# Performance work log

Hardware: AMD Instinct MI355X
Metric: run time of the kernel (lower is better)

Reference implementation:

```python
import jax, jax.numpy as jnp
import numpy as np

B, N, DIM = 4, 2048, 768
HEADS, DH, DEPTH = 12, 64, 4
W = 35                     # hard-coded window size
P = DIM // 2               # window-embedding proj dim
V4 = DIM // 4              # window-embedding value dim
PB = DIM // 4              # dynamic pos-bias MLP width
FF = DIM * 4
NEG = float(np.finfo(np.float32).max)


def setup_inputs() -> dict:
    key = jax.random.key(0)
    ks = iter(jax.random.split(key, 32))
    r = lambda shape: jax.random.normal(next(ks), shape, jnp.float32) * 0.02
    return dict(
        x=jax.random.normal(next(ks), (B, N, DIM), jnp.float32),
        mask=jnp.zeros((B, N), bool),
        ln1_g=jnp.ones((DEPTH, DIM)), ln1_b=jnp.zeros((DEPTH, DIM)),
        qkv_W=r((DEPTH, DIM, 3 * HEADS * DH)),
        temp=jnp.full((DEPTH,), 15.5, jnp.float32),
        we_lin_W=r((DEPTH, DIM, P)), we_q_W=r((DEPTH, P, P)),
        we_k_W=r((DEPTH, DIM, P)), we_v_W=r((DEPTH, DIM, V4)),
        we_bos=jnp.zeros((DEPTH, V4)), we_scale=jnp.ones((DEPTH,)),
        out_W=r((DEPTH, DIM + V4, DIM)),
        ln2_g=jnp.ones((DEPTH, DIM)), ln2_b=jnp.zeros((DEPTH, DIM)),
        glu_W=r((DEPTH, DIM, 2 * FF)), glu_b=jnp.zeros((DEPTH, 2 * FF)),
        ffo_W=r((DEPTH, FF, DIM)), ffo_b=jnp.zeros((DEPTH, DIM)),
        pb_W1=r((1, PB)), pb_b1=jnp.zeros((PB,)),
        pb_W2=r((PB, PB)), pb_b2=jnp.zeros((PB,)),
        pb_W3=r((PB, HEADS)), pb_b3=jnp.zeros((HEADS,)),
    )


def _ln(x, g, b):
    m = x.mean(-1, keepdims=True)
    v = ((x - m) ** 2).mean(-1, keepdims=True)
    return (x - m) * jax.lax.rsqrt(v + 1e-5) * g + b


def _l2norm(t):
    # matches F.normalize(p=2, dim=-1): x / max(||x||, 1e-12)
    return t / jnp.maximum(jnp.linalg.norm(t, axis=-1, keepdims=True), 1e-12)


def _pos_bias(n, W1, b1, W2, b2, W3, b3):
    # DynamicPositionBias(dim=PB, depth=2): Linear->ReLU, Linear->ReLU, Linear
    pos = jnp.arange(-n + 1, n, dtype=jnp.float32)[:, None]          # (2n-1, 1)
    h = jax.nn.relu(pos @ W1 + b1)
    h = jax.nn.relu(h @ W2 + b2)
    out = h @ W3 + b3                                                # (2n-1, H)
    idx = jnp.arange(n)[:, None] - jnp.arange(n)[None, :] + n - 1    # (n, n)
    return jnp.transpose(out[idx], (2, 0, 1))                        # (H, n, n)


def _sinu(n, scale):
    # ScaledSinuEmbedding over proj dim P
    inv = 1.0 / (10000.0 ** (jnp.arange(0, P, 2, dtype=jnp.float32) / P))
    s = jnp.arange(n, dtype=jnp.float32)[:, None] * inv[None, :]
    return jnp.concatenate([jnp.sin(s), jnp.cos(s)], -1) * scale     # (n, P)


def _forward(x, mask, ln1_g, ln1_b, qkv_W, temp, we_lin_W, we_q_W, we_k_W,
             we_v_W, we_bos, we_scale, out_W, ln2_g, ln2_b, glu_W, glu_b,
             ffo_W, ffo_b, pb_W1, pb_b1, pb_W2, pb_b2, pb_W3, pb_b3):
    Bz, Nn, _ = x.shape
    pad = (-Nn) % W
    nw = (Nn + pad) // W
    bias = _pos_bias(W, pb_W1, pb_b1, pb_W2, pb_b2, pb_W3, pb_b3)    # (H, W, W)
    causal = jnp.triu(jnp.ones((W, W), bool), 1)
    mpad = jnp.concatenate([mask, jnp.ones((Bz, pad), bool)], 1).reshape(Bz, nw, W)
    valid = ~mpad                                                    # (B, w, n)
    amask = ~(valid[:, None, :, :, None] & valid[:, None, :, None, :]) | causal
    we_mask = mpad[:, :, None, :]                                    # (B, w, 1, n)
    lengths = jnp.maximum(valid.sum(-1), 1).astype(jnp.float32)[..., None, None]
    sinu35 = _sinu(W, 1.0)                                           # (W, P)

    for l in range(DEPTH):
        # ---- PreNorm + windowed cosine attention ----
        h = _ln(x, ln1_g[l], ln1_b[l])
        hp = jnp.concatenate([h, jnp.zeros((Bz, pad, DIM), h.dtype)], 1)
        hp = hp.reshape(Bz, nw, W, DIM)
        qkv = (hp @ qkv_W[l]).reshape(Bz, nw, W, HEADS, DH, 3)
        q, k, v = (jnp.transpose(qkv[..., i], (0, 3, 1, 2, 4)) for i in range(3))
        q, k = _l2norm(q), _l2norm(k)
        dots = jnp.einsum('bhwid,bhwjd->bhwij', q, k) * temp[l] + bias[None, :, None]
        dots = jnp.where(amask, -NEG, dots)
        attn = jax.nn.softmax(dots, axis=-1)
        o = jnp.einsum('bhwij,bhwjd->bhwid', attn, v)
        o = jnp.transpose(o, (0, 2, 3, 1, 4)).reshape(Bz, nw, W, HEADS * DH)
        # ---- window_embeddings: pooled prev-window embedding attention ----
        we = jnp.where(mpad[..., None], 0.0, o) @ we_lin_W[l]         # (B,w,n,P)
        we = jax.nn.relu(we.sum(-2, keepdims=True) / lengths)        # (B,w,1,P)
        wq = we @ we_q_W[l]
        k2 = o @ we_k_W[l] + sinu35 * we_scale[l]
        v2 = o @ we_v_W[l]
        d2 = jnp.einsum('bwid,bwjd->bwij', wq, k2) * (P ** -0.5)
        d2 = jnp.where(we_mask, -NEG, d2)
        o2 = jnp.einsum('bwij,bwjd->bwid', jax.nn.softmax(d2, -1), v2)  # (B,w,1,V4)
        bos = jnp.broadcast_to(we_bos[l], (Bz, 1, 1, V4))
        o2 = jnp.concatenate([bos, o2], 1)[:, :-1]                   # shift by one window
        o = jnp.concatenate([o, jnp.broadcast_to(o2, (Bz, nw, W, V4))], -1)
        o = (o @ out_W[l]).reshape(Bz, nw * W, DIM)[:, :Nn]
        x = x + o
        # ---- PreNorm + GLU feed-forward ----
        h2 = _ln(x, ln2_g[l], ln2_b[l])
        a, g = jnp.split(h2 @ glu_W[l] + glu_b[l], 2, axis=-1)
        x = x + ((a * jax.nn.silu(g)) @ ffo_W[l] + ffo_b[l])
    return x


def reference(x, mask, ln1_g, ln1_b, qkv_W, temp, we_lin_W, we_q_W, we_k_W,
              we_v_W, we_bos, we_scale, out_W, ln2_g, ln2_b, glu_W, glu_b,
              ffo_W, ffo_b, pb_W1, pb_b1, pb_W2, pb_b2, pb_W3, pb_b3):
    return _forward(x, mask, ln1_g, ln1_b, qkv_W, temp, we_lin_W, we_q_W,
                    we_k_W, we_v_W, we_bos, we_scale, out_W, ln2_g, ln2_b,
                    glu_W, glu_b, ffo_W, ffo_b, pb_W1, pb_b1, pb_W2, pb_b2,
                    pb_W3, pb_b3)
```

## Files before the change

### kernel.cpp

```cpp
#include <hip/hip_runtime.h>
#include <hip/hip_bf16.h>
#include <cstddef>
#include <cstdint>

#define B_ 4
#define N_ 2048
#define DIM_ 768
#define HEADS_ 12
#define DH_ 64
#define DEPTH_ 4
#define W_ 35
#define P_ 384
#define V4_ 192
#define FF_ 3072
#define NW_ 59
#define NPB_ (NW_*W_)
#define NTOK_ (B_*N_)
#define NWB_ (B_*NW_)
#define NTP_ (NWB_*W_)
#define NTPA_ 8448
#define NEG_ 3.402823466e+38f

typedef __bf16 bf16x8 __attribute__((ext_vector_type(8)));
typedef float  f32x4  __attribute__((ext_vector_type(4)));

#define GLOAD16(g, l) __builtin_amdgcn_global_load_lds( \
    (const __attribute__((address_space(1))) uint32_t*)(g), \
    (__attribute__((address_space(3))) uint32_t*)(l), 16, 0, 0)


__global__ __launch_bounds__(192) void posbias1_k(
    const float* __restrict__ W1, const float* __restrict__ b1,
    const float* __restrict__ W2, const float* __restrict__ b2,
    const float* __restrict__ W3, const float* __restrict__ b3,
    float* __restrict__ outk)
{
    __shared__ float h1[192];
    __shared__ float h2[192];
    int i = blockIdx.x;
    int tid = threadIdx.x;
    float pos = (float)(i - 34);
    h1[tid] = fmaxf(pos*W1[tid] + b1[tid], 0.f);
    __syncthreads();
    float s = b2[tid];
    for (int k=0;k<192;k++) s += h1[k]*W2[k*192+tid];
    h2[tid] = fmaxf(s, 0.f);
    __syncthreads();
    if (tid < 12){
        float o = b3[tid];
        for (int k=0;k<192;k++) o += h2[k]*W3[k*12+tid];
        outk[i*12+tid] = o;
    }
}

__global__ void posbias2_k(const float* __restrict__ outk, float* __restrict__ bias)
{
    int e = threadIdx.x + blockIdx.x*blockDim.x;
    if (e >= HEADS_*W_*W_) return;
    int h=e/(W_*W_); int rem=e%(W_*W_); int i=rem/W_; int j=rem%W_;
    bias[e] = outk[(i-j+W_-1)*12 + h];
}

__global__ void sinu_k(float* __restrict__ sinu)
{
    int i = blockIdx.x;
    int k = threadIdx.x;
    float inv = powf(10000.f, -(float)k/192.f);
    float s = (float)i * inv;
    sinu[i*P_ + k]       = sinf(s);
    sinu[i*P_ + 192 + k] = cosf(s);
}

__global__ void len_k(const unsigned char* __restrict__ mask, float* __restrict__ len)
{
    int bw = threadIdx.x + blockIdx.x*blockDim.x;
    if (bw >= NWB_) return;
    int b = bw / NW_, w = bw % NW_;
    int cnt = 0;
    for (int t=0;t<W_;t++){
        int g = w*W_ + t;
        if (g < N_ && mask[b*N_+g]==0) cnt++;
    }
    len[bw] = fmaxf((float)cnt, 1.f);
}

__global__ __launch_bounds__(256) void pack_k(
    const float* __restrict__ W, __bf16* __restrict__ Bp,
    int N, int Ncov, int Nld, size_t lsW, size_t lsB, int qkvperm, int ncol0)
{
    int n = blockIdx.x*256 + threadIdx.x;
    int k8 = blockIdx.y, l = blockIdx.z;
    if (n >= Ncov) return;
    bf16x8 v;
    if (n < N){
        int sn = n;
        if (qkvperm){ int s = n/768, hd = n - s*768; sn = hd*3 + s; }
        const float* w = W + lsW*l + (size_t)k8*8*N + sn;
        #pragma unroll
        for (int e=0;e<8;e++) v[e] = (__bf16)w[(size_t)e*N];
    } else {
        #pragma unroll
        for (int e=0;e<8;e++) v[e] = (__bf16)0.f;
    }
    *(bf16x8*)(Bp + lsB*l + ((size_t)k8*Nld + ncol0 + n)*8) = v;
}

__global__ __launch_bounds__(256) void ln_k(
    const float* __restrict__ x, const float* __restrict__ g,
    const float* __restrict__ b, __bf16* __restrict__ out,
    const float* __restrict__ o2p, int padded)
{
    int r = blockIdx.x;
    int tid = threadIdx.x;
    int lane = tid & 63, wave = tid >> 6;
    int row = r; bool real = true;
    if (padded){
        int bb = r / NPB_, n = r % NPB_;
        if (n >= N_) real = false;
        row = bb*N_ + n;
    }
    float v0=0,v1=0,v2=0;
    if (real){
        const float* xr = x + (size_t)row*DIM_;
        v0 = xr[tid]; v1 = xr[tid+256]; v2 = xr[tid+512];
        if (o2p){
            int bb = row / N_, nn = row % N_;
            const float* op = o2p + (size_t)(bb*NW_ + nn/W_)*DIM_;
            v0 += op[tid]; v1 += op[tid+256]; v2 += op[tid+512];
        }
    }
    float s1 = v0+v1+v2;
    float s2 = v0*v0+v1*v1+v2*v2;
    #pragma unroll
    for (int off=32; off; off>>=1){
        s1 += __shfl_xor(s1, off);
        s2 += __shfl_xor(s2, off);
    }
    __shared__ float a1[4], a2[4];
    if (lane==0){ a1[wave]=s1; a2[wave]=s2; }
    __syncthreads();
    s1 = a1[0]+a1[1]+a1[2]+a1[3];
    s2 = a2[0]+a2[1]+a2[2]+a2[3];
    float m   = s1 * (1.f/768.f);
    float var = s2 * (1.f/768.f) - m*m;
    float inv = rsqrtf(var + 1e-5f);
    __bf16* o = out + (size_t)r*DIM_;
    if (!real){ o[tid]=(__bf16)0.f; o[tid+256]=(__bf16)0.f; o[tid+512]=(__bf16)0.f; return; }
    o[tid]     = (__bf16)((v0-m)*inv*g[tid]     + b[tid]);
    o[tid+256] = (__bf16)((v1-m)*inv*g[tid+256] + b[tid+256]);
    o[tid+512] = (__bf16)((v2-m)*inv*g[tid+512] + b[tid+512]);
}

template<int EPI, bool DUAL, int BM>
__global__ __launch_bounds__(256) void mgemm_k(
    const __bf16* __restrict__ A, const __bf16* __restrict__ Bp,
    float* __restrict__ Cf, __bf16* __restrict__ Cb, float* __restrict__ Cf2,
    float* __restrict__ Cx,
    const float* __restrict__ bias, const float* __restrict__ extra,
    const float* __restrict__ scale_ptr,
    int M, int K, int Nc, int Nld, int Cld)
{
    constexpr int BN = DUAL ? 64 : 128;
    constexpr int RS = BM / 2;
    constexpr int MF = RS / 16;
    constexpr int NF = (BN/2) / 16;
    constexpr int AS = BM * 32;
    constexpr int BS = BN * 32;
    constexpr int ALD = BM / 64;
    constexpr int NL  = ALD + 2;
    __shared__ alignas(16) __bf16 As[3*AS];
    __shared__ alignas(16) __bf16 Bs[3*BS];
    __shared__ alignas(16) __bf16 Gs[DUAL ? 3*BS : 16];
    const int tid = threadIdx.x;
    const int lane = tid & 63, wave = tid >> 6;
    const int wr = wave >> 1, wc = wave & 1;
    const int m0 = blockIdx.y*BM;
    const int n0 = blockIdx.x*BN;
    const int lk = lane >> 4, lr = lane & 15;
    f32x4 acc[MF][NF] = {};
    f32x4 acc2[DUAL?MF:1][NF] = {};

    const __bf16* aP[ALD];
    int aO[ALD];
    #pragma unroll
    for (int q=0;q<ALD;q++){
        int i = tid + q*256;
        int r = i & (BM-1), k8 = i / BM;
        aP[q] = A + (size_t)(m0+r)*K + k8*8;
        aO[q] = i*8;
    }
    const __bf16* bP[2];
    int bO[2];
    if constexpr (!DUAL){
        #pragma unroll
        for (int q=0;q<2;q++){
            int i = tid + q*256;
            int n = i & 127, k8 = i >> 7;
            bP[q] = Bp + ((size_t)k8*Nld + n0 + n)*8;
            bO[q] = i*8;
        }
    } else {
        int n = tid & 63, k8 = tid >> 6;
        bP[0] = Bp + ((size_t)k8*Nld + n0 + n)*8;
        bP[1] = bP[0] + (size_t)FF_*8;
        bO[0] = tid*8;
        bO[1] = tid*8;
    }
    const size_t bStep = (size_t)Nld*32;

    auto stage = [&](int wb){
        #pragma unroll
        for (int q=0;q<ALD;q++)
            GLOAD16(aP[q], As + wb*AS + aO[q]);
        if constexpr (!DUAL){
            GLOAD16(bP[0], Bs + wb*BS + bO[0]);
            GLOAD16(bP[1], Bs + wb*BS + bO[1]);
        } else {
            GLOAD16(bP[0], Bs + wb*BS + bO[0]);
            GLOAD16(bP[1], Gs + wb*BS + bO[1]);
        }
        #pragma unroll
        for (int q=0;q<ALD;q++) aP[q] += 32;
        bP[0] += bStep; bP[1] += bStep;
    };

    const int nk = K >> 5;
    stage(0);
    stage(1);
    int rb = 0;
    for (int t = 0; t < nk; ++t){
        if (t == nk-1)              asm volatile("s_waitcnt vmcnt(0)" ::: "memory");
        else if constexpr (NL == 3) asm volatile("s_waitcnt vmcnt(3)" ::: "memory");
        else                        asm volatile("s_waitcnt vmcnt(4)" ::: "memory");
        __builtin_amdgcn_s_barrier();
        __builtin_amdgcn_sched_barrier(0);
        if (t + 2 < nk){
            int wb = rb + 2; if (wb >= 3) wb -= 3;
            stage(wb);
        }
        const __bf16* as = As + rb*AS + (size_t)(lk*BM + wr*RS + lr)*8;
        const __bf16* bs = Bs + rb*BS + (size_t)(lk*BN + wc*(BN/2) + lr)*8;
        bf16x8 af[MF], bfr[NF];
        #pragma unroll
        for (int m=0;m<MF;m++) af[m] = *(const bf16x8*)(as + m*128);
        #pragma unroll
        for (int n=0;n<NF;n++) bfr[n] = *(const bf16x8*)(bs + n*128);
        __builtin_amdgcn_s_setprio(1);
        #pragma unroll
        for (int m=0;m<MF;m++)
            #pragma unroll
            for (int n=0;n<NF;n++)
                acc[m][n] = __builtin_amdgcn_mfma_f32_16x16x32_bf16(af[m], bfr[n], acc[m][n], 0,0,0);
        if constexpr (DUAL){
            const __bf16* gs = Gs + rb*BS + (size_t)(lk*BN + wc*(BN/2) + lr)*8;
            bf16x8 gfr[NF];
            #pragma unroll
            for (int n=0;n<NF;n++) gfr[n] = *(const bf16x8*)(gs + n*128);
            #pragma unroll
            for (int m=0;m<MF;m++)
                #pragma unroll
                for (int n=0;n<NF;n++)
                    acc2[m][n] = __builtin_amdgcn_mfma_f32_16x16x32_bf16(af[m], gfr[n], acc2[m][n], 0,0,0);
        }
        __builtin_amdgcn_s_setprio(0);
        rb++; if (rb >= 3) rb = 0;
    }

    const int lq = lane >> 4;
    #pragma unroll
    for (int m=0;m<MF;m++){
        #pragma unroll
        for (int r=0;r<4;r++){
            int row = m0 + wr*RS + m*16 + lq*4 + r;
            if (row >= M) continue;
            #pragma unroll
            for (int n=0;n<NF;n++){
                int col = n0 + wc*(BN/2) + n*16 + lr;
                if (col >= Nc) continue;
                float v = acc[m][n][r];
                if (EPI==1){
                    Cb[(size_t)row*Cld + col] = (__bf16)v;
                } else if (EPI==3){
                    int bb = row / N_, nn = row % N_;
                    int bw = bb*NW_ + nn/W_;
                    Cf[(size_t)row*Cld + col] += v + bias[col]
                        + extra[(size_t)bw*DIM_ + col];
                } else if (EPI==4){
                    float a_ = v + bias[col];
                    float g_ = acc2[m][n][r] + bias[col + FF_];
                    Cb[(size_t)row*Cld + col] = (__bf16)(a_ * (g_ / (1.f + expf(-g_))));
                } else if (EPI==8){
                    if (col < P_){
                        int tt = (row % NPB_) % W_;
                        Cf[(size_t)row*P_ + col] = v + extra[tt*P_ + col]*scale_ptr[0];
                    } else if (col < 576){
                        Cf2[(size_t)row*V4_ + (col - P_)] = v;
                    } else {
                        int bb = row / NPB_, nn = row % NPB_;
                        if (nn < N_)
                            Cx[(size_t)(bb*N_ + nn)*DIM_ + (col - 576)] += v;
                    }
                }
            }
        }
    }
}

__global__ __launch_bounds__(256) void gemm0_k(
    const float* __restrict__ A, const float* __restrict__ Bw,
    float* __restrict__ C, int M, int K, int Nc, int ldb)
{
    __shared__ float As[16][65];
    __shared__ float Bs[16][65];
    const int m0 = blockIdx.y*64, n0 = blockIdx.x*64;
    const int tid = threadIdx.x;
    const int ty = tid>>4, tx = tid&15;
    float acc[4][4] = {};
    for (int k0=0; k0<K; k0+=16){
        #pragma unroll
        for (int i=0;i<4;i++){
            int e = tid + i*256;
            int m = e>>4, kk = e&15;
            int mg = m0+m;
            As[kk][m] = (mg < M) ? A[(size_t)mg*K + k0+kk] : 0.f;
        }
        #pragma unroll
        for (int i=0;i<4;i++){
            int e = tid + i*256;
            int kk = e>>6, n = e&63;
            Bs[kk][n] = Bw[(size_t)(k0+kk)*ldb + n0+n];
        }
        __syncthreads();
        #pragma unroll
        for (int kk=0;kk<16;kk++){
            float a[4], bv[4];
            #pragma unroll
            for (int i=0;i<4;i++) a[i] = As[kk][ty*4+i];
            #pragma unroll
            for (int j=0;j<4;j++) bv[j] = Bs[kk][tx*4+j];
            #pragma unroll
            for (int i=0;i<4;i++)
                #pragma unroll
                for (int j=0;j<4;j++) acc[i][j] += a[i]*bv[j];
        }
        __syncthreads();
    }
    #pragma unroll
    for (int i=0;i<4;i++){
        int mg = m0 + ty*4 + i;
        if (mg >= M) continue;
        #pragma unroll
        for (int j=0;j<4;j++){
            int c = n0 + tx*4 + j;
            if (c >= Nc) continue;
            C[(size_t)mg*Nc + c] = acc[i][j];
        }
    }
}

__global__ __launch_bounds__(256) void attn_k(
    const __bf16* __restrict__ qkv, const unsigned char* __restrict__ mask,
    const float* __restrict__ bias, const float* __restrict__ temp_p,
    __bf16* __restrict__ obuf, float* __restrict__ osum)
{
    int bid = blockIdx.x;
    int w = bid % NW_;
    int h = (bid / NW_) % HEADS_;
    int b = bid / (NW_*HEADS_);
    int tid = threadIdx.x;
    __shared__ float qs[W_*DH_], ks[W_*DH_], vs[W_*DH_];
    __shared__ float sc[W_*W_];
    __shared__ float osacc[4][64];
    __shared__ int vf[W_];
    int bw = b*NW_ + w;
    int rbase = bw*W_;
    for (int e=tid; e<W_*DH_; e+=256){
        int t=e>>6, d=e&63;
        size_t idx = (size_t)(rbase+t)*(3*DIM_) + h*DH_ + d;
        qs[e]=(float)qkv[idx];
        ks[e]=(float)qkv[idx+768];
        vs[e]=(float)qkv[idx+1536];
    }
    if (tid < W_){
        int g = w*W_ + tid;
        vf[tid] = (g < N_) && (mask[b*N_+g]==0);
    }
    __syncthreads();
    for (int e=tid; e<2*W_; e+=256){
        float* src = (e<W_)? qs : ks;
        int t = (e<W_)? e : e-W_;
        float s=0;
        for (int d=0;d<DH_;d++){ float v=src[t*DH_+d]; s+=v*v; }
        float inv = 1.f / fmaxf(sqrtf(s), 1e-12f);
        for (int d=0;d<DH_;d++) src[t*DH_+d] *= inv;
    }
    __syncthreads();
    float temp = temp_p[0];
    for (int e=tid; e<W_*W_; e+=256){
        int i=e/W_, j=e%W_;
        float s;
        if (!vf[i] || !vf[j] || j>i) s = -NEG_;
        else {
            float acc=0;
            for (int d=0;d<DH_;d++) acc += qs[i*DH_+d]*ks[j*DH_+d];
            s = acc*temp + bias[(h*W_+i)*W_+j];
        }
        sc[e]=s;
    }
    __syncthreads();
    if (tid < W_){
        int i=tid;
        float mx=-INFINITY;
        for (int j=0;j<W_;j++) mx=fmaxf(mx, sc[i*W_+j]);
        float sum=0;
        for (int j=0;j<W_;j++){ float e_=expf(sc[i*W_+j]-mx); sc[i*W_+j]=e_; sum+=e_; }
        float inv=1.f/sum;
        for (int j=0;j<W_;j++) sc[i*W_+j]*=inv;
    }
    __syncthreads();
    int wavei = tid >> 6, d = tid & 63;
    float psum = 0.f;
    for (int i = wavei; i < W_; i += 4){
        float s=0;
        for (int j=0;j<W_;j++) s += sc[i*W_+j]*vs[j*DH_+d];
        obuf[(size_t)(rbase+i)*DIM_ + h*DH_ + d] = (__bf16)s;
        if (vf[i]) psum += s;
    }
    osacc[wavei][d] = psum;
    __syncthreads();
    if (tid < 64)
        osum[(size_t)bw*DIM_ + h*DH_ + tid] =
            osacc[0][tid]+osacc[1][tid]+osacc[2][tid]+osacc[3][tid];
}

__global__ __launch_bounds__(384) void wefuse_k(
    const float* __restrict__ osum, const float* __restrict__ we_lin,
    const float* __restrict__ we_q, const float* __restrict__ k2,
    const float* __restrict__ v2, const unsigned char* __restrict__ mask,
    const float* __restrict__ len, float* __restrict__ o2)
{
    int bw = blockIdx.x;
    int b = bw / NW_, w = bw % NW_;
    int tid = threadIdx.x;
    __shared__ float osr[768], werr[384], wqr[384], pp[W_];
    osr[tid]     = osum[(size_t)bw*DIM_ + tid];
    osr[tid+384] = osum[(size_t)bw*DIM_ + tid + 384];
    __syncthreads();
    float invlen = 1.f / len[bw];
    float s = 0;
    for (int k=0;k<768;k++) s += osr[k]*we_lin[(size_t)k*P_ + tid];
    werr[tid] = fmaxf(s*invlen, 0.f);
    __syncthreads();
    s = 0;
    for (int k=0;k<384;k++) s += werr[k]*we_q[(size_t)k*P_ + tid];
    wqr[tid] = s;
    __syncthreads();
    if (tid < W_){
        int g = w*W_ + tid;
        bool val = (g < N_) && (mask[b*N_+g]==0);
        float sv = -NEG_;
        if (val){
            float acc=0;
            const float* kr = k2 + (size_t)(bw*W_+tid)*P_;
            for (int c=0;c<P_;c++) acc += wqr[c]*kr[c];
            sv = acc * 0.05103103630798287f;
        }
        pp[tid]=sv;
    }
    __syncthreads();
    if (tid==0){
        float mx=-INFINITY;
        for (int j=0;j<W_;j++) mx=fmaxf(mx,pp[j]);
        float sum=0;
        for (int j=0;j<W_;j++){ float e=expf(pp[j]-mx); pp[j]=e; sum+=e; }
        float inv=1.f/sum;
        for (int j=0;j<W_;j++) pp[j]*=inv;
    }
    __syncthreads();
    if (tid < V4_){
        float sv=0;
        for (int j=0;j<W_;j++) sv += pp[j]*v2[(size_t)(bw*W_+j)*V4_ + tid];
        o2[(size_t)bw*V4_ + tid] = sv;
    }
}

__global__ void o2shift_k(const float* __restrict__ o2, const float* __restrict__ bos,
                          float* __restrict__ o2u)
{
    int e = threadIdx.x + blockIdx.x*blockDim.x;
    if (e >= NWB_*V4_) return;
    int bw = e / V4_, c = e % V4_;
    int w = bw % NW_;
    o2u[e] = (w==0) ? bos[c] : o2[e - V4_];
}


extern "C" void kernel_launch(void* const* d_in, const int* in_sizes, int n_in,
                              void* d_out, int out_size, void* d_ws, size_t ws_size,
                              hipStream_t stream)
{
    const float* x       = (const float*)d_in[0];
    const unsigned char* mask = (const unsigned char*)d_in[1];
    const float* ln1_g   = (const float*)d_in[2];
    const float* ln1_b   = (const float*)d_in[3];
    const float* qkv_W   = (const float*)d_in[4];
    const float* temp    = (const float*)d_in[5];
    const float* we_lin_W= (const float*)d_in[6];
    const float* we_q_W  = (const float*)d_in[7];
    const float* we_k_W  = (const float*)d_in[8];
    const float* we_v_W  = (const float*)d_in[9];
    const float* we_bos  = (const float*)d_in[10];
    const float* we_scale= (const float*)d_in[11];
    const float* out_W   = (const float*)d_in[12];
    const float* ln2_g   = (const float*)d_in[13];
    const float* ln2_b   = (const float*)d_in[14];
    const float* glu_W   = (const float*)d_in[15];
    const float* glu_b   = (const float*)d_in[16];
    const float* ffo_W   = (const float*)d_in[17];
    const float* ffo_b   = (const float*)d_in[18];
    const float* pb_W1   = (const float*)d_in[19];
    const float* pb_b1   = (const float*)d_in[20];
    const float* pb_W2   = (const float*)d_in[21];
    const float* pb_b2   = (const float*)d_in[22];
    const float* pb_W3   = (const float*)d_in[23];
    const float* pb_b3   = (const float*)d_in[24];

    float* xc = (float*)d_out;

    char* p = (char*)d_ws;
    auto alloc = [&](size_t bytes)->char* {
        char* r = p; p += (bytes + 255) & ~(size_t)255; return r;
    };
    float* f_outk = (float*)alloc((size_t)69*12*4);
    float* f_bias = (float*)alloc((size_t)HEADS_*W_*W_*4);
    float* f_sinu = (float*)alloc((size_t)W_*P_*4);
    float* f_len  = (float*)alloc((size_t)NWB_*4);
    float* f_osum = (float*)alloc((size_t)NWB_*DIM_*4);
    float* f_o2   = (float*)alloc((size_t)NWB_*V4_*4);
    float* f_o2u  = (float*)alloc((size_t)NWB_*V4_*4);
    float* f_o2p  = (float*)alloc((size_t)NWB_*DIM_*4);
    __bf16* w_qkv = (__bf16*)alloc((size_t)DEPTH_*96*2304*8*2);
    __bf16* w_kvo = (__bf16*)alloc((size_t)DEPTH_*96*1408*8*2);
    __bf16* w_glu = (__bf16*)alloc((size_t)DEPTH_*96*6144*8*2);
    __bf16* w_ffo = (__bf16*)alloc((size_t)DEPTH_*384*768*8*2);
    char* arena = p;
    __bf16* f_hpad = (__bf16*)alloc((size_t)NTPA_*DIM_*2);
    __bf16* f_qkvb = (__bf16*)alloc((size_t)NTP_*3*DIM_*2);
    __bf16* f_obuf = (__bf16*)alloc((size_t)NTPA_*DIM_*2);
    float*  f_k2   = (float*)alloc((size_t)NTP_*P_*4);
    float*  f_v2   = (float*)alloc((size_t)NTP_*V4_*4);
    __bf16* f_h2 = (__bf16*)arena;
    __bf16* f_ag = (__bf16*)(arena + (((size_t)NTOK_*DIM_*2 + 255) & ~(size_t)255));
    (void)ws_size; (void)in_sizes; (void)n_in; (void)out_size;

    hipMemcpyAsync(xc, x, (size_t)NTOK_*DIM_*sizeof(float),
                   hipMemcpyDeviceToDevice, stream);
    posbias1_k<<<69,192,0,stream>>>(pb_W1,pb_b1,pb_W2,pb_b2,pb_W3,pb_b3,f_outk);
    posbias2_k<<<(HEADS_*W_*W_+255)/256,256,0,stream>>>(f_outk, f_bias);
    sinu_k<<<W_,192,0,stream>>>(f_sinu);
    len_k<<<1,256,0,stream>>>(mask, f_len);
    pack_k<<<dim3(9,96,DEPTH_),256,0,stream>>>(qkv_W, w_qkv, 2304, 2304, 2304,
        (size_t)768*2304, (size_t)96*2304*8, 1, 0);
    pack_k<<<dim3(2,96,DEPTH_),256,0,stream>>>(we_k_W, w_kvo, 384, 384, 1408,
        (size_t)768*384, (size_t)96*1408*8, 0, 0);
    pack_k<<<dim3(1,96,DEPTH_),256,0,stream>>>(we_v_W, w_kvo, 192, 192, 1408,
        (size_t)768*192, (size_t)96*1408*8, 0, 384);
    pack_k<<<dim3(4,96,DEPTH_),256,0,stream>>>(out_W, w_kvo, 768, 832, 1408,
        (size_t)960*768, (size_t)96*1408*8, 0, 576);
    pack_k<<<dim3(24,96,DEPTH_),256,0,stream>>>(glu_W, w_glu, 6144, 6144, 6144,
        (size_t)768*6144, (size_t)96*6144*8, 0, 0);
    pack_k<<<dim3(3,384,DEPTH_),256,0,stream>>>(ffo_W, w_ffo, 768, 768, 768,
        (size_t)3072*768, (size_t)384*768*8, 0, 0);

    for (int l=0;l<DEPTH_;l++){
        ln_k<<<NTP_,256,0,stream>>>(xc, ln1_g+l*DIM_, ln1_b+l*DIM_, f_hpad,
            nullptr, 1);
        mgemm_k<1,false,128><<<dim3(18,65),256,0,stream>>>(f_hpad,
            w_qkv + (size_t)l*96*2304*8, nullptr, f_qkvb, nullptr, nullptr,
            nullptr, nullptr, nullptr, NTP_, DIM_, 3*DIM_, 3*DIM_, 3*DIM_);
        attn_k<<<B_*HEADS_*NW_,256,0,stream>>>(f_qkvb, mask, f_bias, temp+l,
            f_obuf, f_osum);
        mgemm_k<8,false,64><<<dim3(11,130),256,0,stream>>>(f_obuf,
            w_kvo + (size_t)l*96*1408*8, f_k2, nullptr, f_v2, xc,
            nullptr, f_sinu, we_scale+l, NTP_, DIM_, 1344, 1408, 0);
        wefuse_k<<<NWB_,384,0,stream>>>(f_osum, we_lin_W + (size_t)l*DIM_*P_,
            we_q_W + (size_t)l*P_*P_, f_k2, f_v2, mask, f_len, f_o2);
        o2shift_k<<<(NWB_*V4_+255)/256,256,0,stream>>>(f_o2, we_bos+l*V4_, f_o2u);
        gemm0_k<<<dim3(12,4),256,0,stream>>>(f_o2u,
            out_W + (size_t)l*(DIM_+V4_)*DIM_ + (size_t)DIM_*DIM_,
            f_o2p, NWB_, V4_, DIM_, DIM_);

        ln_k<<<NTOK_,256,0,stream>>>(xc, ln2_g+l*DIM_, ln2_b+l*DIM_, f_h2,
            f_o2p, 0);
        mgemm_k<4,true,128><<<dim3(48,64),256,0,stream>>>(f_h2,
            w_glu + (size_t)l*96*6144*8, nullptr, f_ag, nullptr, nullptr,
            glu_b + (size_t)l*2*FF_, nullptr, nullptr,
            NTOK_, DIM_, FF_, 2*FF_, FF_);
        mgemm_k<3,false,64><<<dim3(6,128),256,0,stream>>>(f_ag,
            w_ffo + (size_t)l*384*768*8, xc, nullptr, nullptr, nullptr,
            ffo_b + (size_t)l*DIM_, f_o2p, nullptr,
            NTOK_, FF_, DIM_, DIM_, DIM_);
    }
}
```

Measured before the change: 2.216 ms.

## Enlarge GEMM M-tiles, fold o2 shift into gemm0, pad attention smem

Doubles the BM tile of the KV/out, GLU and FFO GEMMs, halving grid rows so each block reuses its B tile across more rows. A new vmcnt branch handles the extra loads per stage that the larger tile needs. The separate o2shift kernel and its buffer are removed, and gemm0 now reads the shifted o2/bos rows directly. Attention q/k shared arrays get a row stride of 65 to avoid LDS bank conflicts. The larger tiles lower the block count and may hurt occupancy or wave balance on the GPU.

```diff
diff --git a/kernel.cpp b/kernel.cpp
--- a/kernel.cpp
+++ b/kernel.cpp
@@ -20,6 +20,7 @@
 #define NTP_ (NWB_*W_)
 #define NTPA_ 8448
 #define NEG_ 3.402823466e+38f
+#define QLD_ 65
 
 typedef __bf16 bf16x8 __attribute__((ext_vector_type(8)));
 typedef float  f32x4  __attribute__((ext_vector_type(4)));
@@ -231,7 +232,8 @@
     for (int t = 0; t < nk; ++t){
         if (t == nk-1)              asm volatile("s_waitcnt vmcnt(0)" ::: "memory");
         else if constexpr (NL == 3) asm volatile("s_waitcnt vmcnt(3)" ::: "memory");
-        else                        asm volatile("s_waitcnt vmcnt(4)" ::: "memory");
+        else if constexpr (NL == 4) asm volatile("s_waitcnt vmcnt(4)" ::: "memory");
+        else                        asm volatile("s_waitcnt vmcnt(6)" ::: "memory");
         __builtin_amdgcn_s_barrier();
         __builtin_amdgcn_sched_barrier(0);
         if (t + 2 < nk){
@@ -307,8 +309,9 @@
 }
 
 __global__ __launch_bounds__(256) void gemm0_k(
-    const float* __restrict__ A, const float* __restrict__ Bw,
-    float* __restrict__ C, int M, int K, int Nc, int ldb)
+    const float* __restrict__ o2, const float* __restrict__ bos,
+    const float* __restrict__ Bw, float* __restrict__ C,
+    int M, int K, int Nc, int ldb)
 {
     __shared__ float As[16][65];
     __shared__ float Bs[16][65];
@@ -322,7 +325,12 @@
             int e = tid + i*256;
             int m = e>>4, kk = e&15;
             int mg = m0+m;
-            As[kk][m] = (mg < M) ? A[(size_t)mg*K + k0+kk] : 0.f;
+            float v = 0.f;
+            if (mg < M){
+                int w = mg % NW_;
+                v = (w==0) ? bos[k0+kk] : o2[(size_t)(mg-1)*V4_ + k0+kk];
+            }
+            As[kk][m] = v;
         }
         #pragma unroll
         for (int i=0;i<4;i++){
@@ -368,7 +376,7 @@
     int h = (bid / NW_) % HEADS_;
     int b = bid / (NW_*HEADS_);
     int tid = threadIdx.x;
-    __shared__ float qs[W_*DH_], ks[W_*DH_], vs[W_*DH_];
+    __shared__ float qs[W_*QLD_], ks[W_*QLD_], vs[W_*DH_];
     __shared__ float sc[W_*W_];
     __shared__ float osacc[4][64];
     __shared__ int vf[W_];
@@ -377,8 +385,8 @@
     for (int e=tid; e<W_*DH_; e+=256){
         int t=e>>6, d=e&63;
         size_t idx = (size_t)(rbase+t)*(3*DIM_) + h*DH_ + d;
-        qs[e]=(float)qkv[idx];
-        ks[e]=(float)qkv[idx+768];
+        qs[t*QLD_+d]=(float)qkv[idx];
+        ks[t*QLD_+d]=(float)qkv[idx+768];
         vs[e]=(float)qkv[idx+1536];
     }
     if (tid < W_){
@@ -390,9 +398,9 @@
         float* src = (e<W_)? qs : ks;
         int t = (e<W_)? e : e-W_;
         float s=0;
-        for (int d=0;d<DH_;d++){ float v=src[t*DH_+d]; s+=v*v; }
+        for (int d=0;d<DH_;d++){ float v=src[t*QLD_+d]; s+=v*v; }
         float inv = 1.f / fmaxf(sqrtf(s), 1e-12f);
-        for (int d=0;d<DH_;d++) src[t*DH_+d] *= inv;
+        for (int d=0;d<DH_;d++) src[t*QLD_+d] *= inv;
     }
     __syncthreads();
     float temp = temp_p[0];
@@ -402,7 +410,7 @@
         if (!vf[i] || !vf[j] || j>i) s = -NEG_;
         else {
             float acc=0;
-            for (int d=0;d<DH_;d++) acc += qs[i*DH_+d]*ks[j*DH_+d];
+            for (int d=0;d<DH_;d++) acc += qs[i*QLD_+d]*ks[j*QLD_+d];
             s = acc*temp + bias[(h*W_+i)*W_+j];
         }
         sc[e]=s;
@@ -482,16 +490,6 @@
         for (int j=0;j<W_;j++) sv += pp[j]*v2[(size_t)(bw*W_+j)*V4_ + tid];
         o2[(size_t)bw*V4_ + tid] = sv;
     }
-}
-
-__global__ void o2shift_k(const float* __restrict__ o2, const float* __restrict__ bos,
-                          float* __restrict__ o2u)
-{
-    int e = threadIdx.x + blockIdx.x*blockDim.x;
-    if (e >= NWB_*V4_) return;
-    int bw = e / V4_, c = e % V4_;
-    int w = bw % NW_;
-    o2u[e] = (w==0) ? bos[c] : o2[e - V4_];
 }
 
 
@@ -537,7 +535,6 @@
     float* f_len  = (float*)alloc((size_t)NWB_*4);
     float* f_osum = (float*)alloc((size_t)NWB_*DIM_*4);
     float* f_o2   = (float*)alloc((size_t)NWB_*V4_*4);
-    float* f_o2u  = (float*)alloc((size_t)NWB_*V4_*4);
     float* f_o2p  = (float*)alloc((size_t)NWB_*DIM_*4);
     __bf16* w_qkv = (__bf16*)alloc((size_t)DEPTH_*96*2304*8*2);
     __bf16* w_kvo = (__bf16*)alloc((size_t)DEPTH_*96*1408*8*2);
@@ -580,23 +577,22 @@
             nullptr, nullptr, nullptr, NTP_, DIM_, 3*DIM_, 3*DIM_, 3*DIM_);
         attn_k<<<B_*HEADS_*NW_,256,0,stream>>>(f_qkvb, mask, f_bias, temp+l,
             f_obuf, f_osum);
-        mgemm_k<8,false,64><<<dim3(11,130),256,0,stream>>>(f_obuf,
+        mgemm_k<8,false,128><<<dim3(11,65),256,0,stream>>>(f_obuf,
             w_kvo + (size_t)l*96*1408*8, f_k2, nullptr, f_v2, xc,
             nullptr, f_sinu, we_scale+l, NTP_, DIM_, 1344, 1408, 0);
         wefuse_k<<<NWB_,384,0,stream>>>(f_osum, we_lin_W + (size_t)l*DIM_*P_,
             we_q_W + (size_t)l*P_*P_, f_k2, f_v2, mask, f_len, f_o2);
-        o2shift_k<<<(NWB_*V4_+255)/256,256,0,stream>>>(f_o2, we_bos+l*V4_, f_o2u);
-        gemm0_k<<<dim3(12,4),256,0,stream>>>(f_o2u,
+        gemm0_k<<<dim3(12,4),256,0,stream>>>(f_o2, we_bos + (size_t)l*V4_,
             out_W + (size_t)l*(DIM_+V4_)*DIM_ + (size_t)DIM_*DIM_,
             f_o2p, NWB_, V4_, DIM_, DIM_);
 
         ln_k<<<NTOK_,256,0,stream>>>(xc, ln2_g+l*DIM_, ln2_b+l*DIM_, f_h2,
             f_o2p, 0);
-        mgemm_k<4,true,128><<<dim3(48,64),256,0,stream>>>(f_h2,
+        mgemm_k<4,true,256><<<dim3(48,32),256,0,stream>>>(f_h2,
             w_glu + (size_t)l*96*6144*8, nullptr, f_ag, nullptr, nullptr,
             glu_b + (size_t)l*2*FF_, nullptr, nullptr,
             NTOK_, DIM_, FF_, 2*FF_, FF_);
-        mgemm_k<3,false,64><<<dim3(6,128),256,0,stream>>>(f_ag,
+        mgemm_k<3,false,128><<<dim3(6,64),256,0,stream>>>(f_ag,
             w_ffo + (size_t)l*384*768*8, xc, nullptr, nullptr, nullptr,
             ffo_b + (size_t)l*DIM_, f_o2p, nullptr,
             NTOK_, FF_, DIM_, DIM_, DIM_);
```

Measured after the change: 2.908 ms. 31.2% more time.
